# Kernel tuning notes

Hardware: AMD Instinct MI355X
Metric: run time of the kernel (lower is better)

Reference implementation:

```python
import jax, jax.numpy as jnp
import numpy as np

B, C, H, W = 1, 96, 128, 128
P = 4            # patch_size
E = 192          # embed_dim
DI = 384         # d_inner = expand * embed_dim
NS = 16          # d_state
R = 12           # dt_rank = ceil(E/16)
K = 4            # scan directions
NBLK = 8         # SS2D_MBs_num
GW = C // 2      # SCPA group width


def layernorm(x, g, b, eps=1e-5):
    mu = x.mean(-1, keepdims=True)
    v = x.var(-1, keepdims=True)
    return (x - mu) * jax.lax.rsqrt(v + eps) * g + b


def batchnorm(x, g, b, m, v, eps=1e-5):
    # eval-mode BatchNorm2d over channel axis 1 of (B,C,H,W)
    return (x - m[:, None, None]) * jax.lax.rsqrt(v + eps)[:, None, None] * g[:, None, None] + b[:, None, None]


def conv2d(x, w):
    return jax.lax.conv_general_dilated(x, w, (1, 1), 'SAME', dimension_numbers=('NCHW', 'OIHW', 'NCHW'))


def dwconv2d(x, w, b):
    out = jax.lax.conv_general_dilated(x, w[:, None], (1, 1), 'SAME',
                                       dimension_numbers=('NCHW', 'OIHW', 'NCHW'),
                                       feature_group_count=w.shape[0])
    return out + b[None, :, None, None]


def lrelu(x):
    return jnp.where(x >= 0, x, 0.2 * x)


def channel_attention(x, w1, w2):
    # CBAM-style: shared MLP on avg+max pooled channel descriptors, sigmoid gate
    avg = x.mean((2, 3))
    mx = x.max((2, 3))
    mlp = lambda v: jax.nn.relu(v @ w1.T) @ w2.T
    attn = jax.nn.sigmoid(mlp(avg) + mlp(mx))
    return x * attn[:, :, None, None]


def selective_scan(xs, dts, A, Bs, Cs, Dskip):
    # xs,dts: (B,K,DI,L); A: (K,DI,NS); Bs,Cs: (B,K,NS,L); Dskip: (K,DI)
    xs_t = jnp.moveaxis(xs, -1, 0)
    dts_t = jnp.moveaxis(dts, -1, 0)
    Bs_t = jnp.moveaxis(Bs, -1, 0)
    Cs_t = jnp.moveaxis(Cs, -1, 0)
    h0 = jnp.zeros(xs.shape[:3] + (NS,), xs.dtype)  # (B,K,DI,NS)

    def step(h, t):
        xt, dt, Bt, Ct = t
        h = jnp.exp(dt[..., None] * A) * h + (dt * xt)[..., None] * Bt[:, :, None, :]
        return h, jnp.sum(h * Ct[:, :, None, :], axis=-1)

    _, ys = jax.lax.scan(step, h0, (xs_t, dts_t, Bs_t, Cs_t))
    return jnp.moveaxis(ys, 0, -1) + xs * Dskip[None, :, :, None]


def ss2d_block(x, p):
    # VMamba-style VSS block: x + SS2D(LN(x)); x: (B,Hp,Wp,E)
    (ln_g, ln_b, inproj_w, conv_w, conv_b, xproj_w, dtproj_w, dtproj_b,
     Alog, Dskip, on_g, on_b, outproj_w, merge_w) = p
    Bsz, Hp, Wp, _ = x.shape
    L = Hp * Wp
    h = layernorm(x, ln_g, ln_b)
    xz = jnp.einsum('bhwd,ed->bhwe', h, inproj_w)   # (B,Hp,Wp,2*DI)
    xc, z = jnp.split(xz, 2, axis=-1)
    xc = jax.nn.silu(dwconv2d(jnp.transpose(xc, (0, 3, 1, 2)), conv_w, conv_b))  # (B,DI,Hp,Wp)
    # 4-direction cross-scan: row-major, col-major and their reverses
    xf = xc.reshape(Bsz, DI, L)
    xwh = jnp.transpose(xc, (0, 1, 3, 2)).reshape(Bsz, DI, L)
    xs = jnp.stack([xf, xwh, jnp.flip(xf, -1), jnp.flip(xwh, -1)], axis=1)  # (B,K,DI,L)
    x_dbl = jnp.einsum('bkdl,kcd->bkcl', xs, xproj_w)  # (B,K,R+2*NS,L)
    dts, Bm, Cm = jnp.split(x_dbl, [R, R + NS], axis=2)
    dts = jax.nn.softplus(jnp.einsum('bkrl,kdr->bkdl', dts, dtproj_w) + dtproj_b[None, :, :, None])
    A = -jnp.exp(Alog)
    oy = selective_scan(xs, dts, A, Bm, Cm, Dskip)  # (B,K,DI,L)
    y0 = oy[:, 0]
    y1 = jnp.transpose(oy[:, 1].reshape(Bsz, DI, Wp, Hp), (0, 1, 3, 2)).reshape(Bsz, DI, L)
    y2 = jnp.flip(oy[:, 2], -1)
    y3 = jnp.transpose(jnp.flip(oy[:, 3], -1).reshape(Bsz, DI, Wp, Hp), (0, 1, 3, 2)).reshape(Bsz, DI, L)
    y = merge_w[0] * y0 + merge_w[1] * y1 + merge_w[2] * y2 + merge_w[3] * y3  # learnable merge
    y = jnp.transpose(y, (0, 2, 1)).reshape(Bsz, Hp, Wp, DI)
    y = layernorm(y, on_g, on_b) * jax.nn.silu(z)
    return x + jnp.einsum('bhwd,ed->bhwe', y, outproj_w)


def scpa(x, c1a, c1b, k1, k2w, k2b, k3, k4, c3):
    # PAN SCPA: two branches (3x3 conv / pixel-attention conv), 1x1 fuse, residual
    a = lrelu(jnp.einsum('bchw,oc->bohw', x, c1a))
    b = lrelu(jnp.einsum('bchw,oc->bohw', x, c1b))
    a = conv2d(a, k1)
    g = jax.nn.sigmoid(jnp.einsum('bchw,oc->bohw', b, k2w) + k2b[None, :, None, None])
    b = conv2d(conv2d(b, k3) * g, k4)
    out = jnp.einsum('bchw,oc->bohw', jnp.concatenate([lrelu(a), lrelu(b)], 1), c3)
    return out + x


def _forward(x, bn1_g, bn1_b, bn1_m, bn1_v, ca_w1, ca_w2, pe_w, pe_b, pu_w, pu_b,
             blk_ln_g, blk_ln_b, blk_inproj_w, blk_conv_w, blk_conv_b, blk_xproj_w,
             blk_dtproj_w, blk_dtproj_b, blk_Alog, blk_D, blk_on_g, blk_on_b,
             blk_outproj_w, blk_merge_w, bn2_g, bn2_b, bn2_m, bn2_v,
             scpa_c1a_w, scpa_c1b_w, scpa_k1_w, pa_k2_w, pa_k2_b, pa_k3_w, pa_k4_w, scpa_c3_w):
    residual = x
    h = batchnorm(x, bn1_g, bn1_b, bn1_m, bn1_v)
    x1 = channel_attention(h, ca_w1, ca_w2)
    Hp, Wp = H // P, W // P
    # patch embed: (B,C,H,W) -> (B,Hp,Wp,C*P*P) -> linear -> (B,Hp,Wp,E)
    xp = h.reshape(B, C, Hp, P, Wp, P).transpose(0, 2, 4, 1, 3, 5).reshape(B, Hp, Wp, C * P * P)
    x2 = xp @ pe_w.T + pe_b
    blk_params = (blk_ln_g, blk_ln_b, blk_inproj_w, blk_conv_w, blk_conv_b, blk_xproj_w,
                  blk_dtproj_w, blk_dtproj_b, blk_Alog, blk_D, blk_on_g, blk_on_b,
                  blk_outproj_w, blk_merge_w)
    x2, _ = jax.lax.scan(lambda c, p: (ss2d_block(c, p), None), x2, blk_params)
    # patch unembed
    xu = x2 @ pu_w.T + pu_b
    xu = xu.reshape(B, Hp, Wp, C, P, P).transpose(0, 3, 1, 4, 2, 5).reshape(B, C, H, W)
    xsum = residual + x1 + xu
    h2 = batchnorm(xsum, bn2_g, bn2_b, bn2_m, bn2_v)
    out = scpa(h2, scpa_c1a_w, scpa_c1b_w, scpa_k1_w, pa_k2_w, pa_k2_b, pa_k3_w, pa_k4_w, scpa_c3_w)
    return out + xsum


def setup_inputs():
    key = jax.random.key(0)
    kct = [0]
    def nk():
        kct[0] += 1
        return jax.random.fold_in(key, kct[0])
    def nrm(shape, s=0.02):
        return (jax.random.normal(nk(), shape) * s).astype(jnp.float32)
    f32 = jnp.float32
    inp = dict(
        x=jax.random.normal(nk(), (B, C, H, W), dtype=f32),
        bn1_g=jnp.ones((C,), f32), bn1_b=jnp.zeros((C,), f32),
        bn1_m=nrm((C,), 0.05), bn1_v=jnp.ones((C,), f32),
        ca_w1=nrm((C // 16, C), 0.1), ca_w2=nrm((C, C // 16), 0.1),
        pe_w=nrm((E, C * P * P)), pe_b=jnp.zeros((E,), f32),
        pu_w=nrm((C * P * P, E)), pu_b=jnp.zeros((C * P * P,), f32),
        blk_ln_g=jnp.ones((NBLK, E), f32), blk_ln_b=jnp.zeros((NBLK, E), f32),
        blk_inproj_w=nrm((NBLK, 2 * DI, E)),
        blk_conv_w=nrm((NBLK, DI, 3, 3), 0.1),
        blk_conv_b=jnp.zeros((NBLK, DI), f32),
        blk_xproj_w=nrm((NBLK, K, R + 2 * NS, DI)),
        blk_dtproj_w=nrm((NBLK, K, DI, R), 0.1),
        blk_dtproj_b=jnp.full((NBLK, K, DI), -4.6, f32),  # softplus ~= 0.01
        blk_Alog=jnp.broadcast_to(jnp.log(jnp.arange(1, NS + 1, dtype=f32)), (NBLK, K, DI, NS)) + 0.0,
        blk_D=jnp.ones((NBLK, K, DI), f32),
        blk_on_g=jnp.ones((NBLK, DI), f32), blk_on_b=jnp.zeros((NBLK, DI), f32),
        blk_outproj_w=nrm((NBLK, E, DI)),
        blk_merge_w=jnp.ones((NBLK, K), f32),
        bn2_g=jnp.ones((C,), f32), bn2_b=jnp.zeros((C,), f32),
        bn2_m=nrm((C,), 0.05), bn2_v=jnp.ones((C,), f32),
        scpa_c1a_w=nrm((GW, C), 0.05), scpa_c1b_w=nrm((GW, C), 0.05),
        scpa_k1_w=nrm((GW, GW, 3, 3), 0.05),
        pa_k2_w=nrm((GW, GW), 0.05), pa_k2_b=jnp.zeros((GW,), f32),
        pa_k3_w=nrm((GW, GW, 3, 3), 0.05), pa_k4_w=nrm((GW, GW, 3, 3), 0.05),
        scpa_c3_w=nrm((C, 2 * GW), 0.05),
    )
    return inp


def reference(x, bn1_g, bn1_b, bn1_m, bn1_v, ca_w1, ca_w2, pe_w, pe_b, pu_w, pu_b,
              blk_ln_g, blk_ln_b, blk_inproj_w, blk_conv_w, blk_conv_b, blk_xproj_w,
              blk_dtproj_w, blk_dtproj_b, blk_Alog, blk_D, blk_on_g, blk_on_b,
              blk_outproj_w, blk_merge_w, bn2_g, bn2_b, bn2_m, bn2_v,
              scpa_c1a_w, scpa_c1b_w, scpa_k1_w, pa_k2_w, pa_k2_b, pa_k3_w, pa_k4_w, scpa_c3_w):
    return _forward(x, bn1_g, bn1_b, bn1_m, bn1_v, ca_w1, ca_w2, pe_w, pe_b, pu_w, pu_b,
                    blk_ln_g, blk_ln_b, blk_inproj_w, blk_conv_w, blk_conv_b, blk_xproj_w,
                    blk_dtproj_w, blk_dtproj_b, blk_Alog, blk_D, blk_on_g, blk_on_b,
                    blk_outproj_w, blk_merge_w, bn2_g, bn2_b, bn2_m, bn2_v,
                    scpa_c1a_w, scpa_c1b_w, scpa_k1_w, pa_k2_w, pa_k2_b, pa_k3_w, pa_k4_w, scpa_c3_w)
```

## Files before the change

kernel.cpp:

```cpp
#include <hip/hip_runtime.h>
#include <math.h>

#define HW 16384
constexpr int C_ = 96;
constexpr int E_ = 192, DI_ = 384, NS_ = 16, R_ = 12, K_ = 4, NBLK_ = 8, GW_ = 48;
constexpr int L_ = 1024, CXP_ = 44;
constexpr int TC_ = 64;
constexpr int NCH_ = L_ / TC_;

__device__ __forceinline__ float lrelu_(float x){ return x >= 0.f ? x : 0.2f*x; }
__device__ __forceinline__ float sigmoid_(float x){ return 1.f/(1.f+expf(-x)); }
__device__ __forceinline__ float silu_(float x){ return x/(1.f+expf(-x)); }
__device__ __forceinline__ float softplus_(float x){ return fmaxf(x,0.f)+log1pf(expf(-fabsf(x))); }

__global__ void k_transpose(const float* __restrict__ in, float* __restrict__ out,
                            int rows, int cols, int in_stride){
  __shared__ float t[32][33];
  const float* ib = in + (size_t)blockIdx.z*rows*in_stride;
  float* ob = out + (size_t)blockIdx.z*rows*cols;
  int r0 = blockIdx.y*32, c0 = blockIdx.x*32;
  int tx = threadIdx.x, ty = threadIdx.y;
  for (int i=0;i<32;i+=8){
    int r = r0+ty+i, c = c0+tx;
    if (r<rows && c<cols) t[ty+i][tx] = ib[(size_t)r*in_stride+c];
  }
  __syncthreads();
  for (int i=0;i<32;i+=8){
    int c = c0+ty+i, r = r0+tx;
    if (r<rows && c<cols) ob[(size_t)c*rows+r] = t[tx][ty+i];
  }
}

__global__ void k_bn1(const float* __restrict__ x, const float* g, const float* b,
                      const float* m, const float* v,
                      float* __restrict__ h, float* __restrict__ stats){
  int c = blockIdx.x, tid = threadIdx.x;
  float sc = g[c]*rsqrtf(v[c]+1e-5f), sh = b[c]-m[c]*sc;
  const float* xc = x + (size_t)c*HW;
  float* hc = h + (size_t)c*HW;
  float s = 0.f, mx = -1e30f;
  for (int i=tid;i<HW;i+=256){
    float val = fmaf(xc[i], sc, sh);
    hc[i] = val; s += val; mx = fmaxf(mx, val);
  }
  for (int o=32;o;o>>=1){ s += __shfl_xor(s,o); mx = fmaxf(mx, __shfl_xor(mx,o)); }
  __shared__ float ss[4], sm[4];
  int wid = tid>>6, lane = tid&63;
  if (!lane){ ss[wid]=s; sm[wid]=mx; }
  __syncthreads();
  if (!tid){
    stats[c] = (ss[0]+ss[1]+ss[2]+ss[3])*(1.f/HW);
    stats[96+c] = fmaxf(fmaxf(sm[0],sm[1]),fmaxf(sm[2],sm[3]));
  }
}

__global__ void k_attn(const float* __restrict__ stats, const float* __restrict__ w1,
                       const float* __restrict__ w2, float* __restrict__ attn){
  __shared__ float hid[12];
  int tid = threadIdx.x;
  if (tid < 12){
    int j = tid%6, which = tid/6;
    const float* vv = stats + which*96;
    float a = 0.f;
    for (int c=0;c<96;c++) a += vv[c]*w1[j*96+c];
    hid[tid] = fmaxf(a, 0.f);
  }
  __syncthreads();
  if (tid < 96){
    float a = 0.f;
    for (int j=0;j<6;j++) a += (hid[j]+hid[6+j])*w2[tid*6+j];
    attn[tid] = sigmoid_(a);
  }
}

__global__ void k_patchify(const float* __restrict__ h, float* __restrict__ xp){
  int idx = blockIdx.x*256 + threadIdx.x;
  int l = idx/1536, kk = idx%1536;
  int c = kk>>4, i = (kk>>2)&3, j = kk&3;
  int hp = l>>5, wp = l&31;
  xp[idx] = h[((size_t)c<<14) + (size_t)(hp*4+i)*128 + (wp*4+j)];
}

__global__ __launch_bounds__(256) void k_gemm64(const float* __restrict__ act,
                      const float* __restrict__ wt, const float* __restrict__ bias,
                      const float* __restrict__ res, float* __restrict__ out,
                      int K, int N){
  __shared__ float As[16][68];
  __shared__ float Bs[16][64];
  int tid = threadIdx.x;
  int m0 = blockIdx.x*64, n0 = blockIdx.y*64;
  int tx = tid&15, ty = tid>>4;
  int arow = tid>>2, akq = tid&3;
  int brow = tid>>4, bnq = tid&15;
  float4 aR = *(const float4*)&act[(size_t)(m0+arow)*K + akq*4];
  float4 bR = *(const float4*)&wt [(size_t)brow*N + n0 + bnq*4];
  float acc[4][4] = {{0}};
  for (int k0=0; k0<K; k0+=16){
    __syncthreads();
    As[akq*4+0][arow]=aR.x; As[akq*4+1][arow]=aR.y;
    As[akq*4+2][arow]=aR.z; As[akq*4+3][arow]=aR.w;
    *(float4*)&Bs[brow][bnq*4] = bR;
    __syncthreads();
    if (k0+16 < K){
      aR = *(const float4*)&act[(size_t)(m0+arow)*K + k0+16 + akq*4];
      bR = *(const float4*)&wt [(size_t)(k0+16+brow)*N + n0 + bnq*4];
    }
    #pragma unroll
    for (int kk=0; kk<16; kk++){
      float4 av = *(const float4*)&As[kk][ty*4];
      float4 bv = *(const float4*)&Bs[kk][tx*4];
      float aa[4] = {av.x,av.y,av.z,av.w};
      float bb[4] = {bv.x,bv.y,bv.z,bv.w};
      #pragma unroll
      for (int i=0;i<4;i++)
        #pragma unroll
        for (int j=0;j<4;j++) acc[i][j] = fmaf(aa[i], bb[j], acc[i][j]);
    }
  }
  float4 bq = bias ? *(const float4*)&bias[n0+tx*4] : make_float4(0.f,0.f,0.f,0.f);
  #pragma unroll
  for (int i=0;i<4;i++){
    size_t o = (size_t)(m0+ty*4+i)*N + n0 + tx*4;
    float4 r = res ? *(const float4*)&res[o] : make_float4(0.f,0.f,0.f,0.f);
    float4 ov;
    ov.x = acc[i][0]+bq.x+r.x; ov.y = acc[i][1]+bq.y+r.y;
    ov.z = acc[i][2]+bq.z+r.z; ov.w = acc[i][3]+bq.w+r.w;
    *(float4*)&out[o] = ov;
  }
}

__global__ __launch_bounds__(256) void k_gemm32(const float* __restrict__ act,
                      const float* __restrict__ wt, const float* __restrict__ bias,
                      const float* __restrict__ res, float* __restrict__ out,
                      int K, int N){
  __shared__ float As[32][34];
  __shared__ float Bs[32][32];
  int tid = threadIdx.x;
  int m0 = blockIdx.x*32, n0 = blockIdx.y*32;
  int tx = tid&15, ty = tid>>4;
  int arow = tid>>3, akq = tid&7;
  int brow = tid>>3, bn4 = tid&7;
  float4 aR = *(const float4*)&act[(size_t)(m0+arow)*K + akq*4];
  float4 bR = *(const float4*)&wt [(size_t)brow*N + n0 + bn4*4];
  float acc[2][2] = {{0}};
  for (int k0=0; k0<K; k0+=32){
    __syncthreads();
    As[akq*4+0][arow]=aR.x; As[akq*4+1][arow]=aR.y;
    As[akq*4+2][arow]=aR.z; As[akq*4+3][arow]=aR.w;
    *(float4*)&Bs[brow][bn4*4] = bR;
    __syncthreads();
    if (k0+32 < K){
      aR = *(const float4*)&act[(size_t)(m0+arow)*K + k0+32 + akq*4];
      bR = *(const float4*)&wt [(size_t)(k0+32+brow)*N + n0 + bn4*4];
    }
    #pragma unroll
    for (int kk=0; kk<32; kk++){
      float2 av = *(const float2*)&As[kk][ty*2];
      float2 bv = *(const float2*)&Bs[kk][tx*2];
      acc[0][0] = fmaf(av.x, bv.x, acc[0][0]);
      acc[0][1] = fmaf(av.x, bv.y, acc[0][1]);
      acc[1][0] = fmaf(av.y, bv.x, acc[1][0]);
      acc[1][1] = fmaf(av.y, bv.y, acc[1][1]);
    }
  }
  float2 bq = bias ? *(const float2*)&bias[n0+tx*2] : make_float2(0.f,0.f);
  #pragma unroll
  for (int i=0;i<2;i++){
    size_t o = (size_t)(m0+ty*2+i)*N + n0 + tx*2;
    float2 r = res ? *(const float2*)&res[o] : make_float2(0.f,0.f);
    float2 ov;
    ov.x = acc[i][0]+bq.x+r.x; ov.y = acc[i][1]+bq.y+r.y;
    *(float2*)&out[o] = ov;
  }
}

__global__ void k_ln(const float* __restrict__ x, const float* __restrict__ g,
                     const float* __restrict__ b, float* __restrict__ out){
  int l = blockIdx.x*4 + (threadIdx.x>>6);
  int lane = threadIdx.x&63;
  const float* xr = x + (size_t)l*E_;
  float v0 = xr[lane], v1 = xr[lane+64], v2 = xr[lane+128];
  float s = v0+v1+v2, sq = v0*v0+v1*v1+v2*v2;
  for (int o=32;o;o>>=1){ s += __shfl_xor(s,o); sq += __shfl_xor(sq,o); }
  float mu = s*(1.f/192.f);
  float rs = rsqrtf(sq*(1.f/192.f) - mu*mu + 1e-5f);
  float* orow = out + (size_t)l*E_;
  orow[lane]     = (v0-mu)*rs*g[lane]     + b[lane];
  orow[lane+64]  = (v1-mu)*rs*g[lane+64]  + b[lane+64];
  orow[lane+128] = (v2-mu)*rs*g[lane+128] + b[lane+128];
}

__global__ void k_dwconv(const float* __restrict__ xc, const float* __restrict__ w,
                         const float* __restrict__ bias, float* __restrict__ out){
  int d = blockIdx.x;
  const float* in = xc + (size_t)d*L_;
  float wk[9];
  #pragma unroll
  for (int i=0;i<9;i++) wk[i] = w[d*9+i];
  float bb = bias[d];
  for (int p=threadIdx.x; p<L_; p+=256){
    int hh = p>>5, ww = p&31;
    float acc = bb;
    #pragma unroll
    for (int di=0;di<3;di++){
      int y = hh+di-1;
      if ((unsigned)y >= 32u) continue;
      #pragma unroll
      for (int dj=0;dj<3;dj++){
        int xx = ww+dj-1;
        if ((unsigned)xx >= 32u) continue;
        acc = fmaf(in[y*32+xx], wk[di*3+dj], acc);
      }
    }
    out[(size_t)d*L_+p] = silu_(acc);
  }
}

__global__ void k_build_xst(const float* __restrict__ xcs, float* __restrict__ xst){
  __shared__ float t[32][33];
  int d0 = blockIdx.y*32;
  int h0 = blockIdx.x;
  int l0 = h0*32;
  int tx = threadIdx.x, ty = threadIdx.y;
  for (int i=0;i<32;i+=8)
    t[ty+i][tx] = xcs[(size_t)(d0+ty+i)*L_ + l0+tx];
  __syncthreads();
  int d = d0+tx;
  for (int i=0;i<32;i+=8){
    int wq = ty+i;
    int l = l0+wq;
    float val = t[tx][wq];
    int t1 = wq*32 + h0;
    xst[(size_t)l*DI_ + d] = val;
    xst[(size_t)(L_ + t1)*DI_ + d] = val;
    xst[(size_t)(2*L_ + (1023-l))*DI_ + d] = val;
    xst[(size_t)(3*L_ + (1023-t1))*DI_ + d] = val;
  }
}

__global__ __launch_bounds__(256) void k_xdbl(const float* __restrict__ xcs,
                       const float* __restrict__ xw, float* __restrict__ xdbl){
  int k = blockIdx.z;
  int s = blockIdx.x*256 + threadIdx.x;
  int Ts = ((s&31)<<5) | (s>>5);
  int lw;
  if (k==0) lw = s;
  else if (k==1) lw = Ts;
  else if (k==2) lw = 1023-s;
  else lw = 1023-Ts;
  int c0 = blockIdx.y*4;
  const float* w0 = xw + ((size_t)k*CXP_ + c0)*DI_;
  float a0=0,a1=0,a2=0,a3=0;
  const float* src = xcs + s;
  for (int d=0; d<DI_; d++){
    float v = src[(size_t)d*L_];
    a0 = fmaf(v, w0[d],        a0);
    a1 = fmaf(v, w0[DI_+d],    a1);
    a2 = fmaf(v, w0[2*DI_+d],  a2);
    a3 = fmaf(v, w0[3*DI_+d],  a3);
  }
  size_t base = ((size_t)k*CXP_ + c0)*L_ + lw;
  xdbl[base]       = a0;
  xdbl[base+L_]    = a1;
  xdbl[base+2*L_]  = a2;
  xdbl[base+3*L_]  = a3;
}

__global__ void k_dtbc(const float* __restrict__ xdbl, const float* __restrict__ dtw,
                       const float* __restrict__ dtb, float* __restrict__ dts_t,
                       float* __restrict__ bc){
  int k = blockIdx.y, l = blockIdx.x, d = threadIdx.x;
  float acc = dtb[(size_t)k*DI_ + d];
  const float* w = dtw + ((size_t)k*DI_ + d)*R_;
  const float* xr = xdbl + (size_t)k*CXP_*L_ + l;
  #pragma unroll
  for (int r=0;r<R_;r++) acc = fmaf(xr[(size_t)r*L_], w[r], acc);
  dts_t[((size_t)k*L_ + l)*DI_ + d] = softplus_(acc);
  if (d < 32)
    bc[((size_t)k*L_ + l)*32 + d] = xdbl[((size_t)k*CXP_ + R_ + d)*L_ + l];
}

__global__ __launch_bounds__(256) void k_scanA(const float* __restrict__ xst,
                      const float* __restrict__ dts_t, const float* __restrict__ bc,
                      const float* __restrict__ Alog,
                      float* __restrict__ Ech, float* __restrict__ Hch){
  int k = blockIdx.z;
  int d = blockIdx.y*16 + (threadIdx.x>>4);
  int n = threadIdx.x&15;
  int ch = blockIdx.x;
  float A = -expf(Alog[((size_t)k*DI_ + d)*NS_ + n]);
  float aL2 = A * 1.4426950408889634f;
  int t0 = ch*TC_;
  const float* dtp = dts_t + ((size_t)k*L_ + t0)*DI_ + d;
  const float* xp_ = xst   + ((size_t)k*L_ + t0)*DI_ + d;
  const float* bcp = bc    + ((size_t)k*L_ + t0)*32;
  float h = 0.f, Ep = 1.f;
  #pragma unroll 4
  for (int t=0;t<TC_;t++){
    float dt = dtp[(size_t)t*DI_];
    float xv = xp_[(size_t)t*DI_];
    float Bn = bcp[t*32+n];
    float e = exp2f(aL2*dt);
    h = fmaf(e, h, dt*xv*Bn);
    Ep *= e;
  }
  size_t idx = (((size_t)k*NCH_ + ch)*DI_ + d)*NS_ + n;
  Ech[idx] = Ep; Hch[idx] = h;
}

__global__ void k_scanB(const float* __restrict__ Ech, const float* __restrict__ Hch,
                        float* __restrict__ carry){
  int idx = blockIdx.x*256 + threadIdx.x;
  int k = idx / (DI_*NS_);
  int dn = idx % (DI_*NS_);
  float h = 0.f;
  #pragma unroll
  for (int c=0;c<NCH_;c++){
    size_t o = ((size_t)(k*NCH_+c)*DI_*NS_) + dn;
    carry[o] = h;
    h = fmaf(Ech[o], h, Hch[o]);
  }
}

__global__ __launch_bounds__(256) void k_scanC(const float* __restrict__ xst,
                      const float* __restrict__ dts_t, const float* __restrict__ bc,
                      const float* __restrict__ Alog, const float* __restrict__ carry,
                      float* __restrict__ yst){
  int k = blockIdx.z;
  int d = blockIdx.y*16 + (threadIdx.x>>4);
  int n = threadIdx.x&15;
  int ch = blockIdx.x;
  float A = -expf(Alog[((size_t)k*DI_ + d)*NS_ + n]);
  float aL2 = A * 1.4426950408889634f;
  int t0 = ch*TC_;
  const float* dtp = dts_t + ((size_t)k*L_ + t0)*DI_ + d;
  const float* xp_ = xst   + ((size_t)k*L_ + t0)*DI_ + d;
  const float* bcp = bc    + ((size_t)k*L_ + t0)*32;
  float* yp = yst + ((size_t)k*L_ + t0)*DI_ + d;
  float h = carry[(((size_t)k*NCH_ + ch)*DI_ + d)*NS_ + n];
  #pragma unroll 4
  for (int t=0;t<TC_;t++){
    float dt = dtp[(size_t)t*DI_];
    float xv = xp_[(size_t)t*DI_];
    float Bn = bcp[t*32+n], Cn = bcp[t*32+16+n];
    float e = exp2f(aL2*dt);
    h = fmaf(e, h, dt*xv*Bn);
    float p = h*Cn;
    p += __shfl_xor(p,1); p += __shfl_xor(p,2);
    p += __shfl_xor(p,4); p += __shfl_xor(p,8);
    if (n==0) yp[(size_t)t*DI_] = p;
  }
}

__global__ void k_merge(const float* __restrict__ yst, const float* __restrict__ xst,
                        const float* __restrict__ Dsk, const float* __restrict__ mw,
                        const float* __restrict__ ong, const float* __restrict__ onb,
                        const float* __restrict__ xz, float* __restrict__ out){
  int l = blockIdx.x, d = threadIdx.x;
  int T = ((l&31)<<5) | (l>>5);
  int tt[4] = { l, T, 1023-l, 1023-T };
  float v = 0.f;
  #pragma unroll
  for (int k=0;k<4;k++){
    size_t idx = (size_t)(k*L_ + tt[k])*DI_ + d;
    v += mw[k]*(yst[idx] + xst[idx]*Dsk[k*DI_+d]);
  }
  float s = v, sq = v*v;
  for (int o=32;o;o>>=1){ s += __shfl_xor(s,o); sq += __shfl_xor(sq,o); }
  __shared__ float rs_[6], rq_[6];
  int lane = d&63, wid = d>>6;
  if (!lane){ rs_[wid]=s; rq_[wid]=sq; }
  __syncthreads();
  float ts=0.f, tq=0.f;
  #pragma unroll
  for (int i=0;i<6;i++){ ts += rs_[i]; tq += rq_[i]; }
  float mu = ts*(1.f/DI_);
  float rstd = rsqrtf(tq*(1.f/DI_) - mu*mu + 1e-5f);
  float y = (v-mu)*rstd*ong[d] + onb[d];
  float z = xz[(size_t)l*768 + DI_ + d];
  out[(size_t)l*DI_ + d] = y * silu_(z);
}

__global__ void k_sum(const float* __restrict__ x, const float* __restrict__ h,
                      const float* __restrict__ attn, const float* __restrict__ xu,
                      const float* g2, const float* b2, const float* m2, const float* v2,
                      float* __restrict__ xsum, float* __restrict__ h2){
  int idx = blockIdx.x*256 + threadIdx.x;
  int c = idx>>14, p = idx&16383;
  int hh = p>>7, ww = p&127;
  int l = (hh>>2)*32 + (ww>>2);
  int o = (c<<4) + ((hh&3)<<2) + (ww&3);
  float s = x[idx] + h[idx]*attn[c] + xu[(size_t)l*1536 + o];
  xsum[idx] = s;
  h2[idx] = (s - m2[c])*rsqrtf(v2[c]+1e-5f)*g2[c] + b2[c];
}

__global__ __launch_bounds__(256) void k_1x1ab(const float* __restrict__ h2,
                        const float* __restrict__ wa, const float* __restrict__ wb,
                        float* __restrict__ a, float* __restrict__ b){
  __shared__ float lw[96*12];
  int ocg = blockIdx.x;
  for (int i=threadIdx.x; i<96*12; i+=256){
    int o = i%12, c = i/12;
    lw[i] = (o<6) ? wa[(ocg*6 + o)*96 + c] : wb[(ocg*6 + (o-6))*96 + c];
  }
  __syncthreads();
  int p = blockIdx.y*256 + threadIdx.x;
  float acc[12];
  #pragma unroll
  for (int o=0;o<12;o++) acc[o]=0.f;
  for (int c=0;c<96;c++){
    float v = h2[(size_t)c*HW + p];
    const float* w = lw + c*12;
    #pragma unroll
    for (int o=0;o<12;o++) acc[o] = fmaf(v, w[o], acc[o]);
  }
  #pragma unroll
  for (int o=0;o<6;o++){
    a[(size_t)(ocg*6+o)*HW + p] = lrelu_(acc[o]);
    b[(size_t)(ocg*6+o)*HW + p] = lrelu_(acc[6+o]);
  }
}

__global__ __launch_bounds__(256) void k_1x1g(const float* __restrict__ b,
                       const float* __restrict__ w, const float* __restrict__ bias,
                       float* __restrict__ g){
  __shared__ float lw[48*6];
  int ocg = blockIdx.x;
  for (int i=threadIdx.x; i<48*6; i+=256){
    int o = i%6, c = i/6;
    lw[i] = w[(ocg*6 + o)*48 + c];
  }
  __syncthreads();
  int p = blockIdx.y*256 + threadIdx.x;
  float acc[6];
  #pragma unroll
  for (int o=0;o<6;o++) acc[o] = bias[ocg*6+o];
  for (int c=0;c<48;c++){
    float v = b[(size_t)c*HW + p];
    const float* wp = lw + c*6;
    #pragma unroll
    for (int o=0;o<6;o++) acc[o] = fmaf(v, wp[o], acc[o]);
  }
  #pragma unroll
  for (int o=0;o<6;o++) g[(size_t)(ocg*6+o)*HW + p] = sigmoid_(acc[o]);
}

__global__ __launch_bounds__(256) void k_conv3(const float* __restrict__ in,
                        const float* __restrict__ w, const float* __restrict__ aux,
                        float* __restrict__ out, int mode){
  __shared__ float lw[48*9*6];
  int ocg = blockIdx.x;
  for (int i=threadIdx.x; i<48*9*6; i+=256){
    int o = i%6, j = (i/6)%9, ic = i/54;
    lw[i] = w[((size_t)(ocg*6+o)*48 + ic)*9 + j];
  }
  __syncthreads();
  int p = blockIdx.y*256 + threadIdx.x;
  int hh = p>>7, ww = p&127;
  float acc[6];
  #pragma unroll
  for (int o=0;o<6;o++) acc[o]=0.f;
  for (int ic=0; ic<48; ic++){
    const float* ip = in + (size_t)ic*HW;
    float xv[9];
    #pragma unroll
    for (int di=0;di<3;di++){
      int y = hh+di-1;
      bool yok = (unsigned)y < 128u;
      #pragma unroll
      for (int dj=0;dj<3;dj++){
        int xx = ww+dj-1;
        bool ok = yok && ((unsigned)xx < 128u);
        xv[di*3+dj] = ok ? ip[y*128+xx] : 0.f;
      }
    }
    const float* lwp = lw + ic*54;
    #pragma unroll
    for (int j=0;j<9;j++){
      float xj = xv[j];
      const float* wj = lwp + j*6;
      #pragma unroll
      for (int o=0;o<6;o++) acc[o] = fmaf(xj, wj[o], acc[o]);
    }
  }
  #pragma unroll
  for (int o=0;o<6;o++){
    size_t oi = (size_t)(ocg*6+o)*HW + p;
    out[oi] = (mode==0) ? lrelu_(acc[o]) : acc[o]*aux[oi];
  }
}

__global__ __launch_bounds__(256) void k_c3(const float* __restrict__ ab,
                     const float* __restrict__ w, const float* __restrict__ h2,
                     const float* __restrict__ xsum, float* __restrict__ out){
  __shared__ float lw[96*12];
  int ocg = blockIdx.x;
  for (int i=threadIdx.x; i<96*12; i+=256){
    int o = i%12, j = i/12;
    lw[i] = w[(ocg*12 + o)*96 + j];
  }
  __syncthreads();
  int p = blockIdx.y*256 + threadIdx.x;
  float acc[12];
  #pragma unroll
  for (int o=0;o<12;o++) acc[o]=0.f;
  for (int j=0;j<96;j++){
    float v = ab[(size_t)j*HW + p];
    const float* wp = lw + j*12;
    #pragma unroll
    for (int o=0;o<12;o++) acc[o] = fmaf(v, wp[o], acc[o]);
  }
  #pragma unroll
  for (int o=0;o<12;o++){
    size_t oi = (size_t)(ocg*12+o)*HW + p;
    out[oi] = acc[o] + h2[oi] + xsum[oi];
  }
}

extern "C" void kernel_launch(void* const* d_in, const int* in_sizes, int n_in,
                              void* d_out, int out_size, void* d_ws, size_t ws_size,
                              hipStream_t stream){
  (void)in_sizes; (void)n_in; (void)out_size; (void)ws_size;
  const float* x    = (const float*)d_in[0];
  const float* bn1g = (const float*)d_in[1];
  const float* bn1b = (const float*)d_in[2];
  const float* bn1m = (const float*)d_in[3];
  const float* bn1v = (const float*)d_in[4];
  const float* caw1 = (const float*)d_in[5];
  const float* caw2 = (const float*)d_in[6];
  const float* peW  = (const float*)d_in[7];
  const float* peb  = (const float*)d_in[8];
  const float* puW  = (const float*)d_in[9];
  const float* pub  = (const float*)d_in[10];
  const float* lng  = (const float*)d_in[11];
  const float* lnb  = (const float*)d_in[12];
  const float* inW  = (const float*)d_in[13];
  const float* convw= (const float*)d_in[14];
  const float* convb= (const float*)d_in[15];
  const float* xprojw=(const float*)d_in[16];
  const float* dtw  = (const float*)d_in[17];
  const float* dtb  = (const float*)d_in[18];
  const float* Alog = (const float*)d_in[19];
  const float* Dsk  = (const float*)d_in[20];
  const float* ong  = (const float*)d_in[21];
  const float* onb  = (const float*)d_in[22];
  const float* outW = (const float*)d_in[23];
  const float* mw   = (const float*)d_in[24];
  const float* bn2g = (const float*)d_in[25];
  const float* bn2b = (const float*)d_in[26];
  const float* bn2m = (const float*)d_in[27];
  const float* bn2v = (const float*)d_in[28];
  const float* c1a  = (const float*)d_in[29];
  const float* c1b  = (const float*)d_in[30];
  const float* k1w  = (const float*)d_in[31];
  const float* k2w  = (const float*)d_in[32];
  const float* k2b  = (const float*)d_in[33];
  const float* k3w  = (const float*)d_in[34];
  const float* k4w  = (const float*)d_in[35];
  const float* c3w  = (const float*)d_in[36];
  float* out = (float*)d_out;

  float* ws = (float*)d_ws;
  size_t off = 0;
  auto alloc = [&](size_t n){ float* p = ws + off; off += n; return p; };
  float* peWT  = alloc((size_t)1536*192);
  float* puWT  = alloc((size_t)192*1536);
  float* inWT  = alloc((size_t)8*192*768);
  float* outWT = alloc((size_t)8*384*192);
  float* bufH  = alloc((size_t)96*HW);
  float* stats = alloc(256);
  float* attn  = alloc(128);
  float* bufP  = alloc((size_t)1024*1536);
  float* x2a   = alloc((size_t)1024*192);
  float* x2b   = alloc((size_t)1024*192);
  float* bufLN = alloc((size_t)1024*192);
  float* bufXZ = alloc((size_t)1024*768);
  float* bufXC = alloc((size_t)384*1024);
  float* bufXCS= alloc((size_t)384*1024);
  float* bufXST= alloc((size_t)4*1024*384);
  float* xdbl  = alloc((size_t)4*44*1024);
  float* dts   = alloc((size_t)4*1024*384);
  float* bc    = alloc((size_t)4*1024*32);
  float* yst   = alloc((size_t)4*1024*384);
  float* bufY  = alloc((size_t)1024*384);
  float* xsum  = alloc((size_t)96*HW);
  float* h2    = alloc((size_t)96*HW);
  float* Ech   = alloc((size_t)K_*NCH_*DI_*NS_);
  float* Hch   = alloc((size_t)K_*NCH_*DI_*NS_);
  float* carry = alloc((size_t)K_*NCH_*DI_*NS_);

  dim3 tb(32,8);
  k_transpose<<<dim3(48,6,1), tb, 0, stream>>>(peW, peWT, 192, 1536, 1536);
  k_transpose<<<dim3(6,48,1), tb, 0, stream>>>(puW, puWT, 1536, 192, 192);
  k_transpose<<<dim3(6,24,8), tb, 0, stream>>>(inW, inWT, 768, 192, 192);
  k_transpose<<<dim3(12,6,8), tb, 0, stream>>>(outW, outWT, 192, 384, 384);

  k_bn1<<<96,256,0,stream>>>(x, bn1g, bn1b, bn1m, bn1v, bufH, stats);
  k_attn<<<1,128,0,stream>>>(stats, caw1, caw2, attn);
  k_patchify<<<(1024*1536)/256,256,0,stream>>>(bufH, bufP);
  k_gemm32<<<dim3(32,6),256,0,stream>>>(bufP, peWT, peb, nullptr, x2a, 1536, 192);

  float* cur = x2a; float* nxt = x2b;
  for (int b=0;b<8;b++){
    k_ln<<<256,256,0,stream>>>(cur, lng+(size_t)b*192, lnb+(size_t)b*192, bufLN);
    k_gemm64<<<dim3(16,12),256,0,stream>>>(bufLN, inWT+(size_t)b*192*768, nullptr, nullptr, bufXZ, 192, 768);
    k_transpose<<<dim3(12,32,1),tb,0,stream>>>(bufXZ, bufXC, 1024, 384, 768);
    k_dwconv<<<384,256,0,stream>>>(bufXC, convw+(size_t)b*384*9, convb+(size_t)b*384, bufXCS);
    k_build_xst<<<dim3(32,12),tb,0,stream>>>(bufXCS, bufXST);
    k_xdbl<<<dim3(4,11,4),256,0,stream>>>(bufXCS, xprojw+(size_t)b*4*44*384, xdbl);
    k_dtbc<<<dim3(1024,4),384,0,stream>>>(xdbl, dtw+(size_t)b*4*384*12, dtb+(size_t)b*4*384, dts, bc);
    const float* Ab = Alog + (size_t)b*4*384*16;
    k_scanA<<<dim3(NCH_,DI_/16,4),256,0,stream>>>(bufXST, dts, bc, Ab, Ech, Hch);
    k_scanB<<<(K_*DI_*NS_)/256,256,0,stream>>>(Ech, Hch, carry);
    k_scanC<<<dim3(NCH_,DI_/16,4),256,0,stream>>>(bufXST, dts, bc, Ab, carry, yst);
    k_merge<<<1024,384,0,stream>>>(yst, bufXST, Dsk+(size_t)b*4*384, mw+(size_t)b*4,
                                   ong+(size_t)b*384, onb+(size_t)b*384, bufXZ, bufY);
    k_gemm32<<<dim3(32,6),256,0,stream>>>(bufY, outWT+(size_t)b*384*192, nullptr, cur, nxt, 384, 192);
    float* t = cur; cur = nxt; nxt = t;
  }

  k_gemm64<<<dim3(16,24),256,0,stream>>>(cur, puWT, pub, nullptr, bufP, 192, 1536);
  k_sum<<<(96*HW)/256,256,0,stream>>>(x, bufH, attn, bufP, bn2g, bn2b, bn2m, bn2v, xsum, h2);

  float* bufA = dts;
  float* bufB = dts + (size_t)48*HW;
  float* bufG = yst;
  float* bufT = yst + (size_t)48*HW;
  float* ab   = bufXST;
  k_1x1ab<<<dim3(8,64),256,0,stream>>>(h2, c1a, c1b, bufA, bufB);
  k_1x1g<<<dim3(8,64),256,0,stream>>>(bufB, k2w, k2b, bufG);
  k_conv3<<<dim3(8,64),256,0,stream>>>(bufA, k1w, nullptr, ab, 0);
  k_conv3<<<dim3(8,64),256,0,stream>>>(bufB, k3w, bufG, bufT, 1);
  k_conv3<<<dim3(8,64),256,0,stream>>>(bufT, k4w, nullptr, ab+(size_t)48*HW, 0);
  k_c3<<<dim3(8,64),256,0,stream>>>(ab, c3w, h2, xsum, out);
}
```

Before: 1.234 ms.

## Fuse LayerNorm into in-proj GEMM, dwconv with xst build, split-K x-proj

The standalone LayerNorm kernel becomes a per-row stats kernel, and normalization is applied while loading A tiles into a new 32x32 GEMM for the in-projection. The transpose, depthwise conv and direction-stacking kernels merge into one kernel that reads the xz buffer directly through a shared-memory halo. The x-projection is split three ways over the channel dimension to expose more blocks, and dt/bc sums the partial results. The 64-tile GEMM is dropped in favor of the 32-tile GEMM for more blocks. This trades fewer launches and less intermediate traffic for extra partial-sum reads and smaller GEMM tiles with less register reuse.

After: 1.161 ms. -5.9%, faster.

```diff
diff --git a/kernel.cpp b/kernel.cpp
--- a/kernel.cpp
+++ b/kernel.cpp
@@ -79,54 +79,6 @@
   int c = kk>>4, i = (kk>>2)&3, j = kk&3;
   int hp = l>>5, wp = l&31;
   xp[idx] = h[((size_t)c<<14) + (size_t)(hp*4+i)*128 + (wp*4+j)];
-}
-
-__global__ __launch_bounds__(256) void k_gemm64(const float* __restrict__ act,
-                      const float* __restrict__ wt, const float* __restrict__ bias,
-                      const float* __restrict__ res, float* __restrict__ out,
-                      int K, int N){
-  __shared__ float As[16][68];
-  __shared__ float Bs[16][64];
-  int tid = threadIdx.x;
-  int m0 = blockIdx.x*64, n0 = blockIdx.y*64;
-  int tx = tid&15, ty = tid>>4;
-  int arow = tid>>2, akq = tid&3;
-  int brow = tid>>4, bnq = tid&15;
-  float4 aR = *(const float4*)&act[(size_t)(m0+arow)*K + akq*4];
-  float4 bR = *(const float4*)&wt [(size_t)brow*N + n0 + bnq*4];
-  float acc[4][4] = {{0}};
-  for (int k0=0; k0<K; k0+=16){
-    __syncthreads();
-    As[akq*4+0][arow]=aR.x; As[akq*4+1][arow]=aR.y;
-    As[akq*4+2][arow]=aR.z; As[akq*4+3][arow]=aR.w;
-    *(float4*)&Bs[brow][bnq*4] = bR;
-    __syncthreads();
-    if (k0+16 < K){
-      aR = *(const float4*)&act[(size_t)(m0+arow)*K + k0+16 + akq*4];
-      bR = *(const float4*)&wt [(size_t)(k0+16+brow)*N + n0 + bnq*4];
-    }
-    #pragma unroll
-    for (int kk=0; kk<16; kk++){
-      float4 av = *(const float4*)&As[kk][ty*4];
-      float4 bv = *(const float4*)&Bs[kk][tx*4];
-      float aa[4] = {av.x,av.y,av.z,av.w};
-      float bb[4] = {bv.x,bv.y,bv.z,bv.w};
-      #pragma unroll
-      for (int i=0;i<4;i++)
-        #pragma unroll
-        for (int j=0;j<4;j++) acc[i][j] = fmaf(aa[i], bb[j], acc[i][j]);
-    }
-  }
-  float4 bq = bias ? *(const float4*)&bias[n0+tx*4] : make_float4(0.f,0.f,0.f,0.f);
-  #pragma unroll
-  for (int i=0;i<4;i++){
-    size_t o = (size_t)(m0+ty*4+i)*N + n0 + tx*4;
-    float4 r = res ? *(const float4*)&res[o] : make_float4(0.f,0.f,0.f,0.f);
-    float4 ov;
-    ov.x = acc[i][0]+bq.x+r.x; ov.y = acc[i][1]+bq.y+r.y;
-    ov.z = acc[i][2]+bq.z+r.z; ov.w = acc[i][3]+bq.w+r.w;
-    *(float4*)&out[o] = ov;
-  }
 }
 
 __global__ __launch_bounds__(256) void k_gemm32(const float* __restrict__ act,
@@ -174,61 +126,114 @@
   }
 }
 
-__global__ void k_ln(const float* __restrict__ x, const float* __restrict__ g,
-                     const float* __restrict__ b, float* __restrict__ out){
+__global__ void k_lnstats(const float* __restrict__ x, float* __restrict__ mu,
+                          float* __restrict__ rs){
   int l = blockIdx.x*4 + (threadIdx.x>>6);
   int lane = threadIdx.x&63;
   const float* xr = x + (size_t)l*E_;
   float v0 = xr[lane], v1 = xr[lane+64], v2 = xr[lane+128];
   float s = v0+v1+v2, sq = v0*v0+v1*v1+v2*v2;
   for (int o=32;o;o>>=1){ s += __shfl_xor(s,o); sq += __shfl_xor(sq,o); }
-  float mu = s*(1.f/192.f);
-  float rs = rsqrtf(sq*(1.f/192.f) - mu*mu + 1e-5f);
-  float* orow = out + (size_t)l*E_;
-  orow[lane]     = (v0-mu)*rs*g[lane]     + b[lane];
-  orow[lane+64]  = (v1-mu)*rs*g[lane+64]  + b[lane+64];
-  orow[lane+128] = (v2-mu)*rs*g[lane+128] + b[lane+128];
-}
-
-__global__ void k_dwconv(const float* __restrict__ xc, const float* __restrict__ w,
-                         const float* __restrict__ bias, float* __restrict__ out){
-  int d = blockIdx.x;
-  const float* in = xc + (size_t)d*L_;
-  float wk[9];
-  #pragma unroll
-  for (int i=0;i<9;i++) wk[i] = w[d*9+i];
-  float bb = bias[d];
-  for (int p=threadIdx.x; p<L_; p+=256){
-    int hh = p>>5, ww = p&31;
-    float acc = bb;
+  if (!lane){
+    float m = s*(1.f/192.f);
+    mu[l] = m;
+    rs[l] = rsqrtf(sq*(1.f/192.f) - m*m + 1e-5f);
+  }
+}
+
+__global__ __launch_bounds__(256) void k_gemm32ln(const float* __restrict__ act,
+                      const float* __restrict__ wt, const float* __restrict__ lg,
+                      const float* __restrict__ lb, const float* __restrict__ mu,
+                      const float* __restrict__ rs, float* __restrict__ out,
+                      int K, int N){
+  __shared__ float As[32][34];
+  __shared__ float Bs[32][32];
+  int tid = threadIdx.x;
+  int m0 = blockIdx.x*32, n0 = blockIdx.y*32;
+  int tx = tid&15, ty = tid>>4;
+  int arow = tid>>3, akq = tid&7;
+  int brow = tid>>3, bn4 = tid&7;
+  float m = mu[m0+arow], r = rs[m0+arow];
+  float4 aR = *(const float4*)&act[(size_t)(m0+arow)*K + akq*4];
+  float4 gR = *(const float4*)&lg[akq*4];
+  float4 hR = *(const float4*)&lb[akq*4];
+  float4 bR = *(const float4*)&wt[(size_t)brow*N + n0 + bn4*4];
+  float acc[2][2] = {{0}};
+  for (int k0=0; k0<K; k0+=32){
+    __syncthreads();
+    As[akq*4+0][arow] = (aR.x-m)*r*gR.x + hR.x;
+    As[akq*4+1][arow] = (aR.y-m)*r*gR.y + hR.y;
+    As[akq*4+2][arow] = (aR.z-m)*r*gR.z + hR.z;
+    As[akq*4+3][arow] = (aR.w-m)*r*gR.w + hR.w;
+    *(float4*)&Bs[brow][bn4*4] = bR;
+    __syncthreads();
+    if (k0+32 < K){
+      aR = *(const float4*)&act[(size_t)(m0+arow)*K + k0+32 + akq*4];
+      gR = *(const float4*)&lg[k0+32+akq*4];
+      hR = *(const float4*)&lb[k0+32+akq*4];
+      bR = *(const float4*)&wt[(size_t)(k0+32+brow)*N + n0 + bn4*4];
+    }
+    #pragma unroll
+    for (int kk=0; kk<32; kk++){
+      float2 av = *(const float2*)&As[kk][ty*2];
+      float2 bv = *(const float2*)&Bs[kk][tx*2];
+      acc[0][0] = fmaf(av.x, bv.x, acc[0][0]);
+      acc[0][1] = fmaf(av.x, bv.y, acc[0][1]);
+      acc[1][0] = fmaf(av.y, bv.x, acc[1][0]);
+      acc[1][1] = fmaf(av.y, bv.y, acc[1][1]);
+    }
+  }
+  #pragma unroll
+  for (int i=0;i<2;i++){
+    size_t o = (size_t)(m0+ty*2+i)*N + n0 + tx*2;
+    float2 ov; ov.x = acc[i][0]; ov.y = acc[i][1];
+    *(float2*)&out[o] = ov;
+  }
+}
+
+__global__ __launch_bounds__(256) void k_dwxst(const float* __restrict__ xz,
+                        const float* __restrict__ w, const float* __restrict__ bias,
+                        float* __restrict__ xcs, float* __restrict__ xst){
+  __shared__ float ld[96][33];
+  __shared__ float t[32][33];
+  int h0 = blockIdx.x;
+  int d0 = blockIdx.y*32;
+  int tx = threadIdx.x, ty = threadIdx.y;
+  #pragma unroll
+  for (int i=0;i<12;i++){
+    int ll = i*8 + ty;
+    int h = h0 - 1 + (ll>>5);
+    int wv = ll & 31;
+    float v = 0.f;
+    if ((unsigned)h < 32u) v = xz[(size_t)(h*32+wv)*768 + d0 + tx];
+    ld[ll][tx] = v;
+  }
+  __syncthreads();
+  #pragma unroll
+  for (int i=0;i<4;i++){
+    int dl = ty + 8*i;
+    int d = d0 + dl;
+    float acc = bias[d];
+    const float* wp = w + d*9;
     #pragma unroll
     for (int di=0;di<3;di++){
-      int y = hh+di-1;
-      if ((unsigned)y >= 32u) continue;
       #pragma unroll
       for (int dj=0;dj<3;dj++){
-        int xx = ww+dj-1;
-        if ((unsigned)xx >= 32u) continue;
-        acc = fmaf(in[y*32+xx], wk[di*3+dj], acc);
+        int wq = tx + dj - 1;
+        if ((unsigned)wq < 32u)
+          acc = fmaf(ld[di*32 + wq][dl], wp[di*3+dj], acc);
       }
     }
-    out[(size_t)d*L_+p] = silu_(acc);
-  }
-}
-
-__global__ void k_build_xst(const float* __restrict__ xcs, float* __restrict__ xst){
-  __shared__ float t[32][33];
-  int d0 = blockIdx.y*32;
-  int h0 = blockIdx.x;
-  int l0 = h0*32;
-  int tx = threadIdx.x, ty = threadIdx.y;
-  for (int i=0;i<32;i+=8)
-    t[ty+i][tx] = xcs[(size_t)(d0+ty+i)*L_ + l0+tx];
-  __syncthreads();
-  int d = d0+tx;
-  for (int i=0;i<32;i+=8){
-    int wq = ty+i;
-    int l = l0+wq;
+    float val = silu_(acc);
+    xcs[(size_t)d*L_ + h0*32 + tx] = val;
+    t[dl][tx] = val;
+  }
+  __syncthreads();
+  int d = d0 + tx;
+  #pragma unroll
+  for (int i=0;i<4;i++){
+    int wq = ty + 8*i;
+    int l = h0*32 + wq;
     float val = t[tx][wq];
     int t1 = wq*32 + h0;
     xst[(size_t)l*DI_ + d] = val;
@@ -238,9 +243,10 @@
   }
 }
 
-__global__ __launch_bounds__(256) void k_xdbl(const float* __restrict__ xcs,
-                       const float* __restrict__ xw, float* __restrict__ xdbl){
-  int k = blockIdx.z;
+__global__ __launch_bounds__(256) void k_xdblP(const float* __restrict__ xcs,
+                       const float* __restrict__ xw, float* __restrict__ xdblP){
+  int kz = blockIdx.z;
+  int k = kz & 3, sp = kz >> 2;
   int s = blockIdx.x*256 + threadIdx.x;
   int Ts = ((s&31)<<5) | (s>>5);
   int lw;
@@ -249,35 +255,42 @@
   else if (k==2) lw = 1023-s;
   else lw = 1023-Ts;
   int c0 = blockIdx.y*4;
-  const float* w0 = xw + ((size_t)k*CXP_ + c0)*DI_;
+  const float* wp = xw + ((size_t)k*CXP_ + c0)*DI_ + sp*128;
+  const float* src = xcs + s + (size_t)sp*128*L_;
   float a0=0,a1=0,a2=0,a3=0;
-  const float* src = xcs + s;
-  for (int d=0; d<DI_; d++){
+  for (int d=0; d<128; d++){
     float v = src[(size_t)d*L_];
-    a0 = fmaf(v, w0[d],        a0);
-    a1 = fmaf(v, w0[DI_+d],    a1);
-    a2 = fmaf(v, w0[2*DI_+d],  a2);
-    a3 = fmaf(v, w0[3*DI_+d],  a3);
-  }
-  size_t base = ((size_t)k*CXP_ + c0)*L_ + lw;
-  xdbl[base]       = a0;
-  xdbl[base+L_]    = a1;
-  xdbl[base+2*L_]  = a2;
-  xdbl[base+3*L_]  = a3;
-}
-
-__global__ void k_dtbc(const float* __restrict__ xdbl, const float* __restrict__ dtw,
+    a0 = fmaf(v, wp[d],        a0);
+    a1 = fmaf(v, wp[DI_+d],    a1);
+    a2 = fmaf(v, wp[2*DI_+d],  a2);
+    a3 = fmaf(v, wp[3*DI_+d],  a3);
+  }
+  size_t base = (((size_t)sp*4 + k)*CXP_ + c0)*L_ + lw;
+  xdblP[base]       = a0;
+  xdblP[base+L_]    = a1;
+  xdblP[base+2*L_]  = a2;
+  xdblP[base+3*L_]  = a3;
+}
+
+__global__ void k_dtbc(const float* __restrict__ xdblP, const float* __restrict__ dtw,
                        const float* __restrict__ dtb, float* __restrict__ dts_t,
                        float* __restrict__ bc){
   int k = blockIdx.y, l = blockIdx.x, d = threadIdx.x;
+  const float* p0 = xdblP + ((size_t)(0+k)*CXP_)*L_ + l;
+  const float* p1 = xdblP + ((size_t)(4+k)*CXP_)*L_ + l;
+  const float* p2 = xdblP + ((size_t)(8+k)*CXP_)*L_ + l;
   float acc = dtb[(size_t)k*DI_ + d];
   const float* w = dtw + ((size_t)k*DI_ + d)*R_;
-  const float* xr = xdbl + (size_t)k*CXP_*L_ + l;
-  #pragma unroll
-  for (int r=0;r<R_;r++) acc = fmaf(xr[(size_t)r*L_], w[r], acc);
+  #pragma unroll
+  for (int r=0;r<R_;r++){
+    size_t o = (size_t)r*L_;
+    acc = fmaf(p0[o]+p1[o]+p2[o], w[r], acc);
+  }
   dts_t[((size_t)k*L_ + l)*DI_ + d] = softplus_(acc);
-  if (d < 32)
-    bc[((size_t)k*L_ + l)*32 + d] = xdbl[((size_t)k*CXP_ + R_ + d)*L_ + l];
+  if (d < 32){
+    size_t o = (size_t)(R_+d)*L_;
+    bc[((size_t)k*L_ + l)*32 + d] = p0[o]+p1[o]+p2[o];
+  }
 }
 
 __global__ __launch_bounds__(256) void k_scanA(const float* __restrict__ xst,
@@ -574,12 +587,10 @@
   float* bufP  = alloc((size_t)1024*1536);
   float* x2a   = alloc((size_t)1024*192);
   float* x2b   = alloc((size_t)1024*192);
-  float* bufLN = alloc((size_t)1024*192);
   float* bufXZ = alloc((size_t)1024*768);
-  float* bufXC = alloc((size_t)384*1024);
   float* bufXCS= alloc((size_t)384*1024);
   float* bufXST= alloc((size_t)4*1024*384);
-  float* xdbl  = alloc((size_t)4*44*1024);
+  float* xdblP = alloc((size_t)12*44*1024);
   float* dts   = alloc((size_t)4*1024*384);
   float* bc    = alloc((size_t)4*1024*32);
   float* yst   = alloc((size_t)4*1024*384);
@@ -589,6 +600,8 @@
   float* Ech   = alloc((size_t)K_*NCH_*DI_*NS_);
   float* Hch   = alloc((size_t)K_*NCH_*DI_*NS_);
   float* carry = alloc((size_t)K_*NCH_*DI_*NS_);
+  float* muB   = alloc(1024);
+  float* rsB   = alloc(1024);
 
   dim3 tb(32,8);
   k_transpose<<<dim3(48,6,1), tb, 0, stream>>>(peW, peWT, 192, 1536, 1536);
@@ -603,13 +616,13 @@
 
   float* cur = x2a; float* nxt = x2b;
   for (int b=0;b<8;b++){
-    k_ln<<<256,256,0,stream>>>(cur, lng+(size_t)b*192, lnb+(size_t)b*192, bufLN);
-    k_gemm64<<<dim3(16,12),256,0,stream>>>(bufLN, inWT+(size_t)b*192*768, nullptr, nullptr, bufXZ, 192, 768);
-    k_transpose<<<dim3(12,32,1),tb,0,stream>>>(bufXZ, bufXC, 1024, 384, 768);
-    k_dwconv<<<384,256,0,stream>>>(bufXC, convw+(size_t)b*384*9, convb+(size_t)b*384, bufXCS);
-    k_build_xst<<<dim3(32,12),tb,0,stream>>>(bufXCS, bufXST);
-    k_xdbl<<<dim3(4,11,4),256,0,stream>>>(bufXCS, xprojw+(size_t)b*4*44*384, xdbl);
-    k_dtbc<<<dim3(1024,4),384,0,stream>>>(xdbl, dtw+(size_t)b*4*384*12, dtb+(size_t)b*4*384, dts, bc);
+    k_lnstats<<<256,256,0,stream>>>(cur, muB, rsB);
+    k_gemm32ln<<<dim3(32,24),256,0,stream>>>(cur, inWT+(size_t)b*192*768,
+                        lng+(size_t)b*192, lnb+(size_t)b*192, muB, rsB, bufXZ, 192, 768);
+    k_dwxst<<<dim3(32,12),tb,0,stream>>>(bufXZ, convw+(size_t)b*384*9,
+                        convb+(size_t)b*384, bufXCS, bufXST);
+    k_xdblP<<<dim3(4,11,12),256,0,stream>>>(bufXCS, xprojw+(size_t)b*4*44*384, xdblP);
+    k_dtbc<<<dim3(1024,4),384,0,stream>>>(xdblP, dtw+(size_t)b*4*384*12, dtb+(size_t)b*4*384, dts, bc);
     const float* Ab = Alog + (size_t)b*4*384*16;
     k_scanA<<<dim3(NCH_,DI_/16,4),256,0,stream>>>(bufXST, dts, bc, Ab, Ech, Hch);
     k_scanB<<<(K_*DI_*NS_)/256,256,0,stream>>>(Ech, Hch, carry);
@@ -620,7 +633,7 @@
     float* t = cur; cur = nxt; nxt = t;
   }
 
-  k_gemm64<<<dim3(16,24),256,0,stream>>>(cur, puWT, pub, nullptr, bufP, 192, 1536);
+  k_gemm32<<<dim3(32,48),256,0,stream>>>(cur, puWT, pub, nullptr, bufP, 192, 1536);
   k_sum<<<(96*HW)/256,256,0,stream>>>(x, bufH, attn, bufP, bn2g, bn2b, bn2m, bn2v, xsum, h2);
 
   float* bufA = dts;
```
